# Performance work log

Measured on AMD Instinct MI355X. Metric: run time of the kernel, lower is better.

Reference implementation:

```python
import jax, jax.numpy as jnp
import numpy as np

B, N, DIM = 4, 4096, 1024
HEADS, DIM_HEAD = 16, 64
DIM_INNER = HEADS * DIM_HEAD
ATTN_SCALE = 8.0
EPS = 1e-12  # F.normalize default eps


def setup_inputs() -> dict:
    key = jax.random.key(0)
    k1, k2, k3, k4, k5 = jax.random.split(key, 5)
    x = jax.random.normal(k1, (B, N, DIM), dtype=jnp.float32)
    gamma = jnp.ones((DIM,), dtype=jnp.float32)
    # stored as (in, out) so forward is x @ w
    w_qkv = jax.random.normal(k2, (DIM, 3 * DIM_INNER), dtype=jnp.float32) * (DIM ** -0.5)
    temperature = jnp.ones((HEADS, 1, 1), dtype=jnp.float32)
    w_out = jax.random.normal(k3, (DIM_INNER, DIM), dtype=jnp.float32) * (DIM_INNER ** -0.5)
    return {"x": x, "gamma": gamma, "w_qkv": w_qkv, "temperature": temperature, "w_out": w_out}


def _l2norm(t):
    # F.normalize(t, dim=-1): t / max(||t||_2, eps)
    n = jnp.linalg.norm(t, axis=-1, keepdims=True)
    return t / jnp.maximum(n, EPS)


def reference(x, gamma, w_qkv, temperature, w_out):
    b, n, dim = x.shape
    # RMSNorm: F.normalize(x, dim=-1) * sqrt(dim) * gamma
    xn = _l2norm(x) * (dim ** 0.5) * gamma
    # QKV projection -> qkv b h d n
    qkv = (xn @ w_qkv).reshape(b, n, 3, HEADS, DIM_HEAD)
    qkv = qkv.transpose(2, 0, 3, 4, 1)  # (3, b, h, d, n)
    q, k, v = qkv[0], qkv[1], qkv[2]
    # l2-normalize q, k over the sequence (last) axis; temperature-scale q
    q = _l2norm(q) * jnp.exp(temperature)  # temperature: (h,1,1) broadcast
    k = _l2norm(k)
    # cross-covariance attention over the small channel dim d
    sim = jnp.einsum('bhdn,bhen->bhde', q, k) * ATTN_SCALE
    attn = jax.nn.softmax(sim, axis=-1)
    out = jnp.einsum('bhde,bhen->bhdn', attn, v)
    # b h d n -> b n (h d), then out projection
    out = out.transpose(0, 3, 1, 2).reshape(b, n, DIM_INNER)
    return out @ w_out
```

## Files before the change

### kernel.cpp

```cpp
#include <hip/hip_runtime.h>
#include <stdint.h>

typedef unsigned short u16;
typedef unsigned int u32;
typedef __attribute__((ext_vector_type(8))) __bf16 bf16x8;
typedef __attribute__((ext_vector_type(4))) float f32x4;

#define M_TOT 16384
#define DIMX  1024

__device__ __forceinline__ u16 f2b(float f) {
  u32 u = __builtin_bit_cast(u32, f);
  u32 r = (u + 0x7fffu + ((u >> 16) & 1u)) >> 16;
  return (u16)r;
}

__device__ __forceinline__ void gl2lds16(const void* g, void* l) {
  __builtin_amdgcn_global_load_lds((const __attribute__((address_space(1))) void*)g,
                                   (__attribute__((address_space(3))) void*)l,
                                   16, 0, 0);
}

__global__ __launch_bounds__(256) void k_rms(const float* __restrict__ x,
                                             const float* __restrict__ gamma,
                                             u16* __restrict__ xn) {
  int row = blockIdx.x;
  int t = threadIdx.x;
  const float4* xr = (const float4*)(x + (size_t)row * DIMX);
  float4 v = xr[t];
  float ss = v.x * v.x + v.y * v.y + v.z * v.z + v.w * v.w;
#pragma unroll
  for (int o = 32; o > 0; o >>= 1) ss += __shfl_xor(ss, o, 64);
  __shared__ float wss[4];
  int w = t >> 6;
  if ((t & 63) == 0) wss[w] = ss;
  __syncthreads();
  float tot = wss[0] + wss[1] + wss[2] + wss[3];
  float scale = 32.0f / fmaxf(sqrtf(tot), 1e-12f);
  float4 g = ((const float4*)gamma)[t];
  ushort4 o4;
  o4.x = f2b(v.x * scale * g.x);
  o4.y = f2b(v.y * scale * g.y);
  o4.z = f2b(v.z * scale * g.z);
  o4.w = f2b(v.w * scale * g.w);
  ((ushort4*)xn)[(size_t)row * 256 + t] = o4;
}

__global__ __launch_bounds__(256) void k_castT2(const float* __restrict__ wqkv,
                                                const float* __restrict__ wout,
                                                u16* __restrict__ wqT,
                                                u16* __restrict__ woT) {
  __shared__ float tile[32][33];
  const float* in; u16* out; int Cc; int c0;
  if (blockIdx.x < 96) { in = wqkv; out = wqT; Cc = 3072; c0 = blockIdx.x * 32; }
  else                 { in = wout; out = woT; Cc = 1024; c0 = (blockIdx.x - 96) * 32; }
  int r0 = blockIdx.y * 32;
  int tx = threadIdx.x, ty = threadIdx.y;
#pragma unroll
  for (int i = 0; i < 4; i++)
    tile[ty + i * 8][tx] = in[(size_t)(r0 + ty + i * 8) * Cc + c0 + tx];
  __syncthreads();
#pragma unroll
  for (int i = 0; i < 4; i++)
    out[(size_t)(c0 + ty + i * 8) * 1024 + r0 + tx] = f2b(tile[tx][ty + i * 8]);
}


template<bool SWAP>
__device__ __forceinline__ f32x4 mf(bf16x8 a, bf16x8 b, f32x4 c) {
  return SWAP ? __builtin_amdgcn_mfma_f32_16x16x32_bf16(b, a, c, 0, 0, 0)
              : __builtin_amdgcn_mfma_f32_16x16x32_bf16(a, b, c, 0, 0, 0);
}

__device__ __forceinline__ void stage_ab(const u16* __restrict__ Ag,
                                         const u16* __restrict__ Bg,
                                         u16* dstA, u16* dstB, int t, int k0) {
#pragma unroll
  for (int r = 0; r < 2; r++) {
    int c = r * 512 + t;
    int row = c >> 2, s = c & 3;
    int g = s ^ ((row >> 1) & 3);
    gl2lds16(Ag + (size_t)row * 1024 + k0 + g * 8,
             dstA + (r * 512 + (t >> 6) * 64) * 8);
  }
  {
    int row = t >> 2, s = t & 3;
    int g = s ^ ((row >> 1) & 3);
    gl2lds16(Bg + (size_t)row * 1024 + k0 + g * 8,
             dstB + ((t >> 6) * 64) * 8);
  }
}

template<bool SWAP>
__device__ __forceinline__ void gemm_core(const u16* __restrict__ Ag,
                                          const u16* __restrict__ Bg,
                                          u16* lds, int t, f32x4 (&acc)[4][4]) {
  const int lane = t & 63;
  const int r16 = lane & 15, q = lane >> 4;
  const int wr = (t >> 6) >> 1, wc = (t >> 6) & 1;
  const int arow = wr * 64 + r16;
  const int brow = wc * 64 + r16;

  stage_ab(Ag, Bg, lds, lds + 8192, t, 0);
  asm volatile("s_waitcnt vmcnt(0)" ::: "memory");
  __builtin_amdgcn_s_barrier();

  bf16x8 af[4], bf[4];
#pragma unroll 1
  for (int tt = 0; tt < 32; tt++) {
    const int cur = (tt & 1) ? 12288 : 0;
    const int nxt = cur ^ 12288;
    const int k1 = ((tt + 1) & 31) << 5;
    stage_ab(Ag, Bg, lds + nxt, lds + nxt + 8192, t, k1);
    const u16* A = lds + cur;
    const u16* B = lds + cur + 8192;
#pragma unroll
    for (int i = 0; i < 4; i++) {
      int ar = i * 16 + arow;
      int br = i * 16 + brow;
      af[i] = *(const bf16x8*)(A + ar * 32 + (q ^ ((ar >> 1) & 3)) * 8);
      bf[i] = *(const bf16x8*)(B + br * 32 + (q ^ ((br >> 1) & 3)) * 8);
    }
    __builtin_amdgcn_s_setprio(1);
#pragma unroll
    for (int i = 0; i < 4; i++)
#pragma unroll
      for (int j = 0; j < 4; j++)
        acc[i][j] = mf<SWAP>(af[i], bf[j], acc[i][j]);
    __builtin_amdgcn_s_setprio(0);
    asm volatile("s_waitcnt vmcnt(0)" ::: "memory");
    __builtin_amdgcn_s_barrier();
  }
}

__global__ __launch_bounds__(512, 4) void k_gemm1(const u16* __restrict__ A,
                                                  const u16* __restrict__ Bt,
                                                  u16* __restrict__ qkT,
                                                  u16* __restrict__ vmat,
                                                  float* __restrict__ sumsq) {
  __shared__ u16 lds[2 * 12288];
  int l = blockIdx.x;
  int xcd = l & 7, c = l >> 3;
  int mt = xcd * 8 + (c & 7);
  int nt = c >> 3;
  int m0 = mt * 256, n0 = nt * 128;
  int t = threadIdx.x, lane = t & 63;
  int r16 = lane & 15, q = lane >> 4;
  int wr = (t >> 6) >> 1, wc = (t >> 6) & 1;
  f32x4 acc[4][4] = {};
  if (n0 < 2048) {
    gemm_core<false>(A + (size_t)m0 * 1024, Bt + (size_t)n0 * 1024, lds, t, acc);
    int b = m0 >> 12;
#pragma unroll
    for (int j = 0; j < 4; j++) {
      int cc = n0 + wc * 64 + j * 16 + r16;
      float colss = 0.f;
#pragma unroll
      for (int i = 0; i < 4; i++) {
        f32x4 a = acc[i][j];
        colss += a.x * a.x + a.y * a.y + a.z * a.z + a.w * a.w;
        int m = m0 + wr * 64 + i * 16 + q * 4;
        ushort4 o4;
        o4.x = f2b(a.x); o4.y = f2b(a.y); o4.z = f2b(a.z); o4.w = f2b(a.w);
        *(ushort4*)(qkT + (size_t)cc * M_TOT + m) = o4;
      }
      colss += __shfl_xor(colss, 16, 64);
      colss += __shfl_xor(colss, 32, 64);
      if (lane < 16) atomicAdd(&sumsq[b * 2048 + cc], colss);
    }
  } else {
    gemm_core<true>(A + (size_t)m0 * 1024, Bt + (size_t)n0 * 1024, lds, t, acc);
    int vc0 = n0 - 2048;
#pragma unroll
    for (int i = 0; i < 4; i++) {
      int m = m0 + wr * 64 + i * 16 + r16;
#pragma unroll
      for (int j = 0; j < 4; j++) {
        int cc = vc0 + wc * 64 + j * 16 + q * 4;
        f32x4 a = acc[i][j];
        ushort4 o4;
        o4.x = f2b(a.x); o4.y = f2b(a.y); o4.z = f2b(a.z); o4.w = f2b(a.w);
        *(ushort4*)(vmat + (size_t)m * 1024 + cc) = o4;
      }
    }
  }
}

__global__ __launch_bounds__(256) void k_attn_s(const u16* __restrict__ qkT,
                                                float* __restrict__ Spart) {
  __shared__ u16 Ql[64 * 256];
  __shared__ u16 Kl[64 * 256];
  int bh = blockIdx.x, split = blockIdx.y;
  int b = bh >> 4, h = bh & 15;
  int t = threadIdx.x, lane = t & 63, w = t >> 6;
  int r16 = lane & 15, q = lane >> 4;
  const u16* qbase = qkT + (size_t)(h * 64) * M_TOT + b * 4096 + split * 1024;
  const u16* kbase = qkT + (size_t)(1024 + h * 64) * M_TOT + b * 4096 + split * 1024;
  int drow = w * 16 + r16;
  f32x4 acc[4] = {};
#pragma unroll 1
  for (int it = 0; it < 4; it++) {
    int ncol = it * 256;
#pragma unroll
    for (int r = 0; r < 8; r++) {
      int ch = r * 256 + t;
      int row = ch >> 5;
      int sl = (ch & 31) ^ (row & 31);
      gl2lds16(qbase + (size_t)row * M_TOT + ncol + sl * 8,
               Ql + (r * 256 + w * 64) * 8);
      gl2lds16(kbase + (size_t)row * M_TOT + ncol + sl * 8,
               Kl + (r * 256 + w * 64) * 8);
    }
    asm volatile("s_waitcnt vmcnt(0)" ::: "memory");
    __syncthreads();
#pragma unroll
    for (int it2 = 0; it2 < 8; it2++) {
      bf16x8 aq = *(const bf16x8*)(Ql + drow * 256 + (((it2 * 4 + q) ^ (drow & 31)) * 8));
#pragma unroll
      for (int j = 0; j < 4; j++) {
        int erow = j * 16 + r16;
        bf16x8 bk = *(const bf16x8*)(Kl + erow * 256 + (((it2 * 4 + q) ^ (erow & 31)) * 8));
        acc[j] = __builtin_amdgcn_mfma_f32_16x16x32_bf16(bk, aq, acc[j], 0, 0, 0);
      }
    }
    __syncthreads();
  }
  float* Sp = Spart + ((size_t)split * 64 + bh) * 4096;
#pragma unroll
  for (int j = 0; j < 4; j++)
    *(f32x4*)(Sp + drow * 64 + j * 16 + q * 4) = acc[j];
}

__global__ __launch_bounds__(256) void k_softmax(const float* __restrict__ Spart,
                                                 const float* __restrict__ sumsq,
                                                 const float* __restrict__ temp,
                                                 u16* __restrict__ PT) {
  int bh = blockIdx.x;
  int b = bh >> 4, h = bh & 15;
  int t = threadIdx.x;
  int d = t & 63, w = t >> 6;
  int e0 = w * 16;
  __shared__ float rnk[64];
  __shared__ float redm[4][64];
  __shared__ float reds[4][64];
  if (t < 64) rnk[t] = 1.0f / fmaxf(sqrtf(sumsq[b * 2048 + 1024 + h * 64 + t]), 1e-12f);
  __syncthreads();
  float nq = sqrtf(sumsq[b * 2048 + h * 64 + d]);
  float qs = 8.0f * __expf(temp[h]) / fmaxf(nq, 1e-12f);
  const float* Sp = Spart + (size_t)bh * 4096 + d * 64 + e0;
  float vals[16];
#pragma unroll
  for (int e = 0; e < 16; e += 4) {
    f32x4 v = {};
#pragma unroll
    for (int s = 0; s < 4; s++)
      v += *(const f32x4*)(Sp + (size_t)s * 64 * 4096 + e);
    vals[e + 0] = v.x; vals[e + 1] = v.y; vals[e + 2] = v.z; vals[e + 3] = v.w;
  }
  float mx = -3.0e38f;
#pragma unroll
  for (int e = 0; e < 16; e++) {
    float v = vals[e] * qs * rnk[e0 + e];
    vals[e] = v;
    mx = fmaxf(mx, v);
  }
  redm[w][d] = mx;
  __syncthreads();
  float M = fmaxf(fmaxf(redm[0][d], redm[1][d]), fmaxf(redm[2][d], redm[3][d]));
  float s = 0.f;
#pragma unroll
  for (int e = 0; e < 16; e++) {
    float v = __expf(vals[e] - M);
    vals[e] = v;
    s += v;
  }
  reds[w][d] = s;
  __syncthreads();
  float inv = 1.0f / (reds[0][d] + reds[1][d] + reds[2][d] + reds[3][d]);
#pragma unroll
  for (int e = 0; e < 16; e++)
    PT[((size_t)bh * 64 + e0 + e) * 64 + d] = f2b(vals[e] * inv);
}

__global__ __launch_bounds__(256) void k_m(const u16* __restrict__ woT,
                                           const u16* __restrict__ PT,
                                           u16* __restrict__ MT) {
  int bh = blockIdx.x;
  int b = bh >> 4, h = bh & 15;
  int o0 = blockIdx.y * 128;
  int t = threadIdx.x, lane = t & 63, w = t >> 6;
  int r16 = lane & 15, q = lane >> 4;
  const u16* pbase = PT + (size_t)bh * 4096;
  f32x4 acc[2][4] = {};
#pragma unroll
  for (int ks = 0; ks < 2; ks++) {
    int kk = ks * 32 + q * 8;
    bf16x8 af[2], bfr[4];
#pragma unroll
    for (int i = 0; i < 2; i++)
      af[i] = *(const bf16x8*)(woT + (size_t)(o0 + w * 32 + i * 16 + r16) * 1024 + h * 64 + kk);
#pragma unroll
    for (int j = 0; j < 4; j++)
      bfr[j] = *(const bf16x8*)(pbase + (size_t)(j * 16 + r16) * 64 + kk);
#pragma unroll
    for (int i = 0; i < 2; i++)
#pragma unroll
      for (int j = 0; j < 4; j++)
        acc[i][j] = __builtin_amdgcn_mfma_f32_16x16x32_bf16(af[i], bfr[j], acc[i][j], 0, 0, 0);
  }
  u16* dst = MT + (size_t)b * 1024 * 1024;
#pragma unroll
  for (int i = 0; i < 2; i++) {
    int o = o0 + w * 32 + i * 16 + q * 4;
#pragma unroll
    for (int j = 0; j < 4; j++) {
      int e = h * 64 + j * 16 + r16;
      f32x4 a = acc[i][j];
      dst[(size_t)(o + 0) * 1024 + e] = f2b(a.x);
      dst[(size_t)(o + 1) * 1024 + e] = f2b(a.y);
      dst[(size_t)(o + 2) * 1024 + e] = f2b(a.z);
      dst[(size_t)(o + 3) * 1024 + e] = f2b(a.w);
    }
  }
}

__global__ __launch_bounds__(512, 4) void k_gemm2(const u16* __restrict__ A,
                                                  const u16* __restrict__ Bt,
                                                  float* __restrict__ C) {
  __shared__ u16 lds[2 * 12288];
  int l = blockIdx.x;
  int xcd = l & 7, c = l >> 3;
  int mt = xcd * 8 + (c & 7);
  int nt = c >> 3;
  int m0 = mt * 256, n0 = nt * 128;
  int b = m0 >> 12;
  const u16* Bb = Bt + (size_t)b * 1024 * 1024;
  int t = threadIdx.x, lane = t & 63;
  int r16 = lane & 15, q = lane >> 4;
  int wr = (t >> 6) >> 1, wc = (t >> 6) & 1;
  f32x4 acc[4][4] = {};
  gemm_core<true>(A + (size_t)m0 * 1024, Bb + (size_t)n0 * 1024, lds, t, acc);
#pragma unroll
  for (int i = 0; i < 4; i++) {
    int m = m0 + wr * 64 + i * 16 + r16;
#pragma unroll
    for (int j = 0; j < 4; j++) {
      int cc = n0 + wc * 64 + j * 16 + q * 4;
      *(f32x4*)(C + (size_t)m * 1024 + cc) = acc[i][j];
    }
  }
}

extern "C" void kernel_launch(void* const* d_in, const int* in_sizes, int n_in,
                              void* d_out, int out_size, void* d_ws, size_t ws_size,
                              hipStream_t stream) {
  const float* x     = (const float*)d_in[0];
  const float* gamma = (const float*)d_in[1];
  const float* wqkv  = (const float*)d_in[2];
  const float* temp  = (const float*)d_in[3];
  const float* wout  = (const float*)d_in[4];
  float* out = (float*)d_out;

  char* ws = (char*)d_ws;
  size_t off = 0;
  u16* xn = (u16*)(ws + off);    off += (size_t)M_TOT * 1024 * 2;
  u16* wqT = (u16*)(ws + off);   off += (size_t)3072 * 1024 * 2;
  u16* woT = (u16*)(ws + off);   off += (size_t)1024 * 1024 * 2;
  u16* qkT = (u16*)(ws + off);   off += (size_t)2048 * M_TOT * 2;
  u16* vmat = (u16*)(ws + off);  off += (size_t)M_TOT * 1024 * 2;
  float* sumsq = (float*)(ws + off); off += (size_t)4 * 2048 * 4;
  u16* PT = (u16*)(ws + off);    off += (size_t)64 * 64 * 64 * 2;
  u16* MT = (u16*)(ws + off);    off += (size_t)4 * 1024 * 1024 * 2;

  float* Spart = (float*)xn;

  hipMemsetAsync((void*)sumsq, 0, (size_t)4 * 2048 * 4, stream);

  k_rms<<<16384, 256, 0, stream>>>(x, gamma, xn);
  dim3 cb(32, 8);
  k_castT2<<<dim3(128, 32), cb, 0, stream>>>(wqkv, wout, wqT, woT);
  k_gemm1<<<1536, 512, 0, stream>>>(xn, wqT, qkT, vmat, sumsq);
  k_attn_s<<<dim3(64, 4), 256, 0, stream>>>(qkT, Spart);
  k_softmax<<<64, 256, 0, stream>>>(Spart, sumsq, temp, PT);
  k_m<<<dim3(64, 8), 256, 0, stream>>>(woT, PT, MT);
  k_gemm2<<<512, 512, 0, stream>>>(vmat, MT, out);
}
```

Measured before the change: 326.3 us.

## Fuse all stages into one persistent kernel with grid-wide barriers

Replaces seven separate kernel launches with a single persistent 512-block kernel. Stages are separated by a software grid barrier, an atomic counter with spin-wait. The attention-score stage is re-split into 16 partial sums so all 512 blocks have work. Softmax and the P·Wout product are fused, keeping P in LDS instead of a global buffer. The aim is to remove launch gaps and tail effects between stages, at the cost of relying on all 512 blocks being co-resident, idle blocks during small stages, and a 3-tile-per-block loop for the first GEMM.

```diff
diff --git a/kernel.cpp b/kernel.cpp
--- a/kernel.cpp
+++ b/kernel.cpp
@@ -8,6 +8,7 @@
 
 #define M_TOT 16384
 #define DIMX  1024
+#define NBLK  512
 
 __device__ __forceinline__ u16 f2b(float f) {
   u32 u = __builtin_bit_cast(u32, f);
@@ -21,50 +22,16 @@
                                    16, 0, 0);
 }
 
-__global__ __launch_bounds__(256) void k_rms(const float* __restrict__ x,
-                                             const float* __restrict__ gamma,
-                                             u16* __restrict__ xn) {
-  int row = blockIdx.x;
-  int t = threadIdx.x;
-  const float4* xr = (const float4*)(x + (size_t)row * DIMX);
-  float4 v = xr[t];
-  float ss = v.x * v.x + v.y * v.y + v.z * v.z + v.w * v.w;
-#pragma unroll
-  for (int o = 32; o > 0; o >>= 1) ss += __shfl_xor(ss, o, 64);
-  __shared__ float wss[4];
-  int w = t >> 6;
-  if ((t & 63) == 0) wss[w] = ss;
+__device__ __forceinline__ void gsync(u32* cnt, u32 thresh) {
+  __threadfence();
   __syncthreads();
-  float tot = wss[0] + wss[1] + wss[2] + wss[3];
-  float scale = 32.0f / fmaxf(sqrtf(tot), 1e-12f);
-  float4 g = ((const float4*)gamma)[t];
-  ushort4 o4;
-  o4.x = f2b(v.x * scale * g.x);
-  o4.y = f2b(v.y * scale * g.y);
-  o4.z = f2b(v.z * scale * g.z);
-  o4.w = f2b(v.w * scale * g.w);
-  ((ushort4*)xn)[(size_t)row * 256 + t] = o4;
-}
-
-__global__ __launch_bounds__(256) void k_castT2(const float* __restrict__ wqkv,
-                                                const float* __restrict__ wout,
-                                                u16* __restrict__ wqT,
-                                                u16* __restrict__ woT) {
-  __shared__ float tile[32][33];
-  const float* in; u16* out; int Cc; int c0;
-  if (blockIdx.x < 96) { in = wqkv; out = wqT; Cc = 3072; c0 = blockIdx.x * 32; }
-  else                 { in = wout; out = woT; Cc = 1024; c0 = (blockIdx.x - 96) * 32; }
-  int r0 = blockIdx.y * 32;
-  int tx = threadIdx.x, ty = threadIdx.y;
-#pragma unroll
-  for (int i = 0; i < 4; i++)
-    tile[ty + i * 8][tx] = in[(size_t)(r0 + ty + i * 8) * Cc + c0 + tx];
+  if (threadIdx.x == 0) {
+    atomicAdd(cnt, 1u);
+    while (atomicAdd(cnt, 0u) < thresh) __builtin_amdgcn_s_sleep(2);
+  }
   __syncthreads();
-#pragma unroll
-  for (int i = 0; i < 4; i++)
-    out[(size_t)(c0 + ty + i * 8) * 1024 + r0 + tx] = f2b(tile[tx][ty + i * 8]);
-}
-
+  __threadfence();
+}
 
 template<bool SWAP>
 __device__ __forceinline__ f32x4 mf(bf16x8 a, bf16x8 b, f32x4 c) {
@@ -133,220 +100,276 @@
   }
 }
 
-__global__ __launch_bounds__(512, 4) void k_gemm1(const u16* __restrict__ A,
-                                                  const u16* __restrict__ Bt,
-                                                  u16* __restrict__ qkT,
-                                                  u16* __restrict__ vmat,
-                                                  float* __restrict__ sumsq) {
-  __shared__ u16 lds[2 * 12288];
-  int l = blockIdx.x;
-  int xcd = l & 7, c = l >> 3;
-  int mt = xcd * 8 + (c & 7);
-  int nt = c >> 3;
-  int m0 = mt * 256, n0 = nt * 128;
-  int t = threadIdx.x, lane = t & 63;
-  int r16 = lane & 15, q = lane >> 4;
-  int wr = (t >> 6) >> 1, wc = (t >> 6) & 1;
-  f32x4 acc[4][4] = {};
-  if (n0 < 2048) {
-    gemm_core<false>(A + (size_t)m0 * 1024, Bt + (size_t)n0 * 1024, lds, t, acc);
+__global__ __launch_bounds__(512, 4) void k_mega(
+    const float* __restrict__ x, const float* __restrict__ gamma,
+    const float* __restrict__ wqkv, const float* __restrict__ wout,
+    const float* __restrict__ temp,
+    u16* __restrict__ xn, u16* __restrict__ wqT, u16* __restrict__ woT,
+    u16* __restrict__ qkT, u16* __restrict__ vmat,
+    float* __restrict__ sumsq, u16* __restrict__ MT,
+    float* __restrict__ Spart, float* __restrict__ out, u32* cnt) {
+  __shared__ __align__(16) char smem[65536];
+  const int t = threadIdx.x;
+  const int blk = blockIdx.x;
+  const int lane = t & 63;
+  const int r16 = lane & 15, q = lane >> 4;
+
+  {
+    float* tile = (float*)smem;
+    float* wss  = (float*)(smem + 8448);
+    int vb = t >> 8;
+    int tl = t & 255;
+#pragma unroll 1
+    for (int i = 0; i < 20; i++) {
+      int v = blk * 2 + vb + i * 1024;
+      if (v < 16384) {
+        const float4* xr = (const float4*)(x + (size_t)v * DIMX);
+        float4 vv = xr[tl];
+        float ss = vv.x * vv.x + vv.y * vv.y + vv.z * vv.z + vv.w * vv.w;
+#pragma unroll
+        for (int o = 32; o > 0; o >>= 1) ss += __shfl_xor(ss, o, 64);
+        if ((tl & 63) == 0) wss[vb * 4 + (tl >> 6)] = ss;
+        __syncthreads();
+        float tot = wss[vb * 4 + 0] + wss[vb * 4 + 1] + wss[vb * 4 + 2] + wss[vb * 4 + 3];
+        float scale = 32.0f / fmaxf(sqrtf(tot), 1e-12f);
+        float4 g = ((const float4*)gamma)[tl];
+        ushort4 o4;
+        o4.x = f2b(vv.x * scale * g.x);
+        o4.y = f2b(vv.y * scale * g.y);
+        o4.z = f2b(vv.z * scale * g.z);
+        o4.w = f2b(vv.w * scale * g.w);
+        ((ushort4*)xn)[(size_t)v * 256 + tl] = o4;
+      } else {
+        int bb = v - 16384;
+        int bx = bb & 127, by = bb >> 7;
+        int r0 = by * 32;
+        int tx = tl & 31, ty = tl >> 5;
+        const float* in; u16* outp; int Cc, c0;
+        if (bx < 96) { in = wqkv; outp = wqT; Cc = 3072; c0 = bx * 32; }
+        else         { in = wout; outp = woT; Cc = 1024; c0 = (bx - 96) * 32; }
+        float* tl2 = tile + vb * 32 * 33;
+#pragma unroll
+        for (int i2 = 0; i2 < 4; i2++)
+          tl2[(ty + i2 * 8) * 33 + tx] = in[(size_t)(r0 + ty + i2 * 8) * Cc + c0 + tx];
+        __syncthreads();
+#pragma unroll
+        for (int i2 = 0; i2 < 4; i2++)
+          outp[(size_t)(c0 + ty + i2 * 8) * 1024 + r0 + tx] = f2b(tl2[tx * 33 + ty + i2 * 8]);
+      }
+      __syncthreads();
+    }
+  }
+  gsync(cnt, NBLK);
+
+  {
+    u16* lds = (u16*)smem;
+#pragma unroll 1
+    for (int i = 0; i < 3; i++) {
+      int l = blk + i * NBLK;
+      int xcd = l & 7, c = l >> 3;
+      int mt = xcd * 8 + (c & 7);
+      int nt = c >> 3;
+      int m0 = mt * 256, n0 = nt * 128;
+      int wr = (t >> 6) >> 1, wc = (t >> 6) & 1;
+      f32x4 acc[4][4] = {};
+      if (n0 < 2048) {
+        gemm_core<false>(xn + (size_t)m0 * 1024, wqT + (size_t)n0 * 1024, lds, t, acc);
+        int b = m0 >> 12;
+#pragma unroll
+        for (int j = 0; j < 4; j++) {
+          int cc = n0 + wc * 64 + j * 16 + r16;
+          float colss = 0.f;
+#pragma unroll
+          for (int i2 = 0; i2 < 4; i2++) {
+            f32x4 a = acc[i2][j];
+            colss += a.x * a.x + a.y * a.y + a.z * a.z + a.w * a.w;
+            int m = m0 + wr * 64 + i2 * 16 + q * 4;
+            ushort4 o4;
+            o4.x = f2b(a.x); o4.y = f2b(a.y); o4.z = f2b(a.z); o4.w = f2b(a.w);
+            *(ushort4*)(qkT + (size_t)cc * M_TOT + m) = o4;
+          }
+          colss += __shfl_xor(colss, 16, 64);
+          colss += __shfl_xor(colss, 32, 64);
+          if (lane < 16) atomicAdd(&sumsq[b * 2048 + cc], colss);
+        }
+      } else {
+        gemm_core<true>(xn + (size_t)m0 * 1024, wqT + (size_t)n0 * 1024, lds, t, acc);
+        int vc0 = n0 - 2048;
+#pragma unroll
+        for (int i2 = 0; i2 < 4; i2++) {
+          int m = m0 + wr * 64 + i2 * 16 + r16;
+#pragma unroll
+          for (int j = 0; j < 4; j++) {
+            int cc = vc0 + wc * 64 + j * 16 + q * 4;
+            f32x4 a = acc[i2][j];
+            ushort4 o4;
+            o4.x = f2b(a.x); o4.y = f2b(a.y); o4.z = f2b(a.z); o4.w = f2b(a.w);
+            *(ushort4*)(vmat + (size_t)m * 1024 + cc) = o4;
+          }
+        }
+      }
+    }
+  }
+  gsync(cnt, 2 * NBLK);
+
+  {
+    u16* Ql = (u16*)smem;
+    u16* Kl = (u16*)smem + 16384;
+    int bh = blk & 63, split = blk >> 6;
+    int b = bh >> 4, h = bh & 15;
+    int w = t >> 6, wl = w & 3, wg = w >> 2;
+    const u16* qbase = qkT + (size_t)(h * 64) * M_TOT + b * 4096 + split * 512;
+    const u16* kbase = qkT + (size_t)(1024 + h * 64) * M_TOT + b * 4096 + split * 512;
+    int drow = wl * 16 + r16;
+    f32x4 acc[4] = {};
+#pragma unroll 1
+    for (int it = 0; it < 2; it++) {
+      int ncol = it * 256;
+#pragma unroll
+      for (int r = 0; r < 4; r++) {
+        int ch = r * 512 + t;
+        int row = ch >> 5;
+        int sl = (ch & 31) ^ (row & 31);
+        gl2lds16(qbase + (size_t)row * M_TOT + ncol + sl * 8,
+                 Ql + (r * 512 + w * 64) * 8);
+        gl2lds16(kbase + (size_t)row * M_TOT + ncol + sl * 8,
+                 Kl + (r * 512 + w * 64) * 8);
+      }
+      asm volatile("s_waitcnt vmcnt(0)" ::: "memory");
+      __syncthreads();
+#pragma unroll
+      for (int h2 = 0; h2 < 4; h2++) {
+        int it2 = h2 * 2 + wg;
+        bf16x8 aq = *(const bf16x8*)(Ql + drow * 256 + (((it2 * 4 + q) ^ (drow & 31)) * 8));
+#pragma unroll
+        for (int j = 0; j < 4; j++) {
+          int erow = j * 16 + r16;
+          bf16x8 bk = *(const bf16x8*)(Kl + erow * 256 + (((it2 * 4 + q) ^ (erow & 31)) * 8));
+          acc[j] = __builtin_amdgcn_mfma_f32_16x16x32_bf16(bk, aq, acc[j], 0, 0, 0);
+        }
+      }
+      __syncthreads();
+    }
+    int sp = split * 2 + wg;
+    float* Sp = Spart + ((size_t)sp * 64 + bh) * 4096;
+#pragma unroll
+    for (int j = 0; j < 4; j++)
+      *(f32x4*)(Sp + drow * 64 + j * 16 + q * 4) = acc[j];
+  }
+  gsync(cnt, 3 * NBLK);
+
+  if (blk < 64) {
+    u16* PT_lds = (u16*)smem;
+    float* rnk  = (float*)(smem + 8192);
+    float* redm = (float*)(smem + 8448);
+    float* reds = (float*)(smem + 10496);
+    int bh = blk;
+    int b = bh >> 4, h = bh & 15;
+    int d = t & 63, w = t >> 6;
+    int e0 = w * 8;
+    if (t < 64) rnk[t] = 1.0f / fmaxf(sqrtf(sumsq[b * 2048 + 1024 + h * 64 + t]), 1e-12f);
+    __syncthreads();
+    float nq = sqrtf(sumsq[b * 2048 + h * 64 + d]);
+    float qs = 8.0f * __expf(temp[h]) / fmaxf(nq, 1e-12f);
+    float vals[8];
+#pragma unroll
+    for (int e = 0; e < 8; e += 4) {
+      f32x4 v = {};
+#pragma unroll
+      for (int s = 0; s < 16; s++)
+        v += *(const f32x4*)(Spart + ((size_t)s * 64 + bh) * 4096 + d * 64 + e0 + e);
+      vals[e + 0] = v.x; vals[e + 1] = v.y; vals[e + 2] = v.z; vals[e + 3] = v.w;
+    }
+    float mx = -3.0e38f;
+#pragma unroll
+    for (int e = 0; e < 8; e++) {
+      float v = vals[e] * qs * rnk[e0 + e];
+      vals[e] = v;
+      mx = fmaxf(mx, v);
+    }
+    redm[w * 64 + d] = mx;
+    __syncthreads();
+    float M = redm[d];
+#pragma unroll
+    for (int k = 1; k < 8; k++) M = fmaxf(M, redm[k * 64 + d]);
+    float ssum = 0.f;
+#pragma unroll
+    for (int e = 0; e < 8; e++) {
+      float v = __expf(vals[e] - M);
+      vals[e] = v;
+      ssum += v;
+    }
+    reds[w * 64 + d] = ssum;
+    __syncthreads();
+    float tot = reds[d];
+#pragma unroll
+    for (int k = 1; k < 8; k++) tot += reds[k * 64 + d];
+    float inv = 1.0f / tot;
+#pragma unroll
+    for (int e = 0; e < 8; e++)
+      PT_lds[(e0 + e) * 64 + d] = f2b(vals[e] * inv);
+    __syncthreads();
+    int tl = t & 255, vb = t >> 8;
+    int lane2 = tl & 63, w4 = tl >> 6;
+    int r2 = lane2 & 15, q2 = lane2 >> 4;
+    u16* dst = MT + (size_t)b * 1024 * 1024;
+#pragma unroll 1
+    for (int ot = vb; ot < 8; ot += 2) {
+      int o0 = ot * 128;
+      f32x4 acc2[2][4] = {};
+#pragma unroll
+      for (int ks = 0; ks < 2; ks++) {
+        int kk = ks * 32 + q2 * 8;
+        bf16x8 af[2], bfr[4];
+#pragma unroll
+        for (int i = 0; i < 2; i++)
+          af[i] = *(const bf16x8*)(woT + (size_t)(o0 + w4 * 32 + i * 16 + r2) * 1024 + h * 64 + kk);
+#pragma unroll
+        for (int j = 0; j < 4; j++)
+          bfr[j] = *(const bf16x8*)(PT_lds + (size_t)(j * 16 + r2) * 64 + kk);
+#pragma unroll
+        for (int i = 0; i < 2; i++)
+#pragma unroll
+          for (int j = 0; j < 4; j++)
+            acc2[i][j] = __builtin_amdgcn_mfma_f32_16x16x32_bf16(af[i], bfr[j], acc2[i][j], 0, 0, 0);
+      }
+#pragma unroll
+      for (int i = 0; i < 2; i++) {
+        int o = o0 + w4 * 32 + i * 16 + q2 * 4;
+#pragma unroll
+        for (int j = 0; j < 4; j++) {
+          int e = h * 64 + j * 16 + r2;
+          f32x4 a = acc2[i][j];
+          dst[(size_t)(o + 0) * 1024 + e] = f2b(a.x);
+          dst[(size_t)(o + 1) * 1024 + e] = f2b(a.y);
+          dst[(size_t)(o + 2) * 1024 + e] = f2b(a.z);
+          dst[(size_t)(o + 3) * 1024 + e] = f2b(a.w);
+        }
+      }
+    }
+  }
+  gsync(cnt, 4 * NBLK);
+
+  {
+    u16* lds = (u16*)smem;
+    int l = blk;
+    int xcd = l & 7, c = l >> 3;
+    int mt = xcd * 8 + (c & 7);
+    int nt = c >> 3;
+    int m0 = mt * 256, n0 = nt * 128;
     int b = m0 >> 12;
-#pragma unroll
-    for (int j = 0; j < 4; j++) {
-      int cc = n0 + wc * 64 + j * 16 + r16;
-      float colss = 0.f;
-#pragma unroll
-      for (int i = 0; i < 4; i++) {
-        f32x4 a = acc[i][j];
-        colss += a.x * a.x + a.y * a.y + a.z * a.z + a.w * a.w;
-        int m = m0 + wr * 64 + i * 16 + q * 4;
-        ushort4 o4;
-        o4.x = f2b(a.x); o4.y = f2b(a.y); o4.z = f2b(a.z); o4.w = f2b(a.w);
-        *(ushort4*)(qkT + (size_t)cc * M_TOT + m) = o4;
-      }
-      colss += __shfl_xor(colss, 16, 64);
-      colss += __shfl_xor(colss, 32, 64);
-      if (lane < 16) atomicAdd(&sumsq[b * 2048 + cc], colss);
-    }
-  } else {
-    gemm_core<true>(A + (size_t)m0 * 1024, Bt + (size_t)n0 * 1024, lds, t, acc);
-    int vc0 = n0 - 2048;
+    int wr = (t >> 6) >> 1, wc = (t >> 6) & 1;
+    f32x4 acc[4][4] = {};
+    gemm_core<true>(vmat + (size_t)m0 * 1024,
+                    MT + (size_t)b * 1048576 + (size_t)n0 * 1024, lds, t, acc);
 #pragma unroll
     for (int i = 0; i < 4; i++) {
       int m = m0 + wr * 64 + i * 16 + r16;
 #pragma unroll
       for (int j = 0; j < 4; j++) {
-        int cc = vc0 + wc * 64 + j * 16 + q * 4;
-        f32x4 a = acc[i][j];
-        ushort4 o4;
-        o4.x = f2b(a.x); o4.y = f2b(a.y); o4.z = f2b(a.z); o4.w = f2b(a.w);
-        *(ushort4*)(vmat + (size_t)m * 1024 + cc) = o4;
-      }
-    }
-  }
-}
-
-__global__ __launch_bounds__(256) void k_attn_s(const u16* __restrict__ qkT,
-                                                float* __restrict__ Spart) {
-  __shared__ u16 Ql[64 * 256];
-  __shared__ u16 Kl[64 * 256];
-  int bh = blockIdx.x, split = blockIdx.y;
-  int b = bh >> 4, h = bh & 15;
-  int t = threadIdx.x, lane = t & 63, w = t >> 6;
-  int r16 = lane & 15, q = lane >> 4;
-  const u16* qbase = qkT + (size_t)(h * 64) * M_TOT + b * 4096 + split * 1024;
-  const u16* kbase = qkT + (size_t)(1024 + h * 64) * M_TOT + b * 4096 + split * 1024;
-  int drow = w * 16 + r16;
-  f32x4 acc[4] = {};
-#pragma unroll 1
-  for (int it = 0; it < 4; it++) {
-    int ncol = it * 256;
-#pragma unroll
-    for (int r = 0; r < 8; r++) {
-      int ch = r * 256 + t;
-      int row = ch >> 5;
-      int sl = (ch & 31) ^ (row & 31);
-      gl2lds16(qbase + (size_t)row * M_TOT + ncol + sl * 8,
-               Ql + (r * 256 + w * 64) * 8);
-      gl2lds16(kbase + (size_t)row * M_TOT + ncol + sl * 8,
-               Kl + (r * 256 + w * 64) * 8);
-    }
-    asm volatile("s_waitcnt vmcnt(0)" ::: "memory");
-    __syncthreads();
-#pragma unroll
-    for (int it2 = 0; it2 < 8; it2++) {
-      bf16x8 aq = *(const bf16x8*)(Ql + drow * 256 + (((it2 * 4 + q) ^ (drow & 31)) * 8));
-#pragma unroll
-      for (int j = 0; j < 4; j++) {
-        int erow = j * 16 + r16;
-        bf16x8 bk = *(const bf16x8*)(Kl + erow * 256 + (((it2 * 4 + q) ^ (erow & 31)) * 8));
-        acc[j] = __builtin_amdgcn_mfma_f32_16x16x32_bf16(bk, aq, acc[j], 0, 0, 0);
-      }
-    }
-    __syncthreads();
-  }
-  float* Sp = Spart + ((size_t)split * 64 + bh) * 4096;
-#pragma unroll
-  for (int j = 0; j < 4; j++)
-    *(f32x4*)(Sp + drow * 64 + j * 16 + q * 4) = acc[j];
-}
-
-__global__ __launch_bounds__(256) void k_softmax(const float* __restrict__ Spart,
-                                                 const float* __restrict__ sumsq,
-                                                 const float* __restrict__ temp,
-                                                 u16* __restrict__ PT) {
-  int bh = blockIdx.x;
-  int b = bh >> 4, h = bh & 15;
-  int t = threadIdx.x;
-  int d = t & 63, w = t >> 6;
-  int e0 = w * 16;
-  __shared__ float rnk[64];
-  __shared__ float redm[4][64];
-  __shared__ float reds[4][64];
-  if (t < 64) rnk[t] = 1.0f / fmaxf(sqrtf(sumsq[b * 2048 + 1024 + h * 64 + t]), 1e-12f);
-  __syncthreads();
-  float nq = sqrtf(sumsq[b * 2048 + h * 64 + d]);
-  float qs = 8.0f * __expf(temp[h]) / fmaxf(nq, 1e-12f);
-  const float* Sp = Spart + (size_t)bh * 4096 + d * 64 + e0;
-  float vals[16];
-#pragma unroll
-  for (int e = 0; e < 16; e += 4) {
-    f32x4 v = {};
-#pragma unroll
-    for (int s = 0; s < 4; s++)
-      v += *(const f32x4*)(Sp + (size_t)s * 64 * 4096 + e);
-    vals[e + 0] = v.x; vals[e + 1] = v.y; vals[e + 2] = v.z; vals[e + 3] = v.w;
-  }
-  float mx = -3.0e38f;
-#pragma unroll
-  for (int e = 0; e < 16; e++) {
-    float v = vals[e] * qs * rnk[e0 + e];
-    vals[e] = v;
-    mx = fmaxf(mx, v);
-  }
-  redm[w][d] = mx;
-  __syncthreads();
-  float M = fmaxf(fmaxf(redm[0][d], redm[1][d]), fmaxf(redm[2][d], redm[3][d]));
-  float s = 0.f;
-#pragma unroll
-  for (int e = 0; e < 16; e++) {
-    float v = __expf(vals[e] - M);
-    vals[e] = v;
-    s += v;
-  }
-  reds[w][d] = s;
-  __syncthreads();
-  float inv = 1.0f / (reds[0][d] + reds[1][d] + reds[2][d] + reds[3][d]);
-#pragma unroll
-  for (int e = 0; e < 16; e++)
-    PT[((size_t)bh * 64 + e0 + e) * 64 + d] = f2b(vals[e] * inv);
-}
-
-__global__ __launch_bounds__(256) void k_m(const u16* __restrict__ woT,
-                                           const u16* __restrict__ PT,
-                                           u16* __restrict__ MT) {
-  int bh = blockIdx.x;
-  int b = bh >> 4, h = bh & 15;
-  int o0 = blockIdx.y * 128;
-  int t = threadIdx.x, lane = t & 63, w = t >> 6;
-  int r16 = lane & 15, q = lane >> 4;
-  const u16* pbase = PT + (size_t)bh * 4096;
-  f32x4 acc[2][4] = {};
-#pragma unroll
-  for (int ks = 0; ks < 2; ks++) {
-    int kk = ks * 32 + q * 8;
-    bf16x8 af[2], bfr[4];
-#pragma unroll
-    for (int i = 0; i < 2; i++)
-      af[i] = *(const bf16x8*)(woT + (size_t)(o0 + w * 32 + i * 16 + r16) * 1024 + h * 64 + kk);
-#pragma unroll
-    for (int j = 0; j < 4; j++)
-      bfr[j] = *(const bf16x8*)(pbase + (size_t)(j * 16 + r16) * 64 + kk);
-#pragma unroll
-    for (int i = 0; i < 2; i++)
-#pragma unroll
-      for (int j = 0; j < 4; j++)
-        acc[i][j] = __builtin_amdgcn_mfma_f32_16x16x32_bf16(af[i], bfr[j], acc[i][j], 0, 0, 0);
-  }
-  u16* dst = MT + (size_t)b * 1024 * 1024;
-#pragma unroll
-  for (int i = 0; i < 2; i++) {
-    int o = o0 + w * 32 + i * 16 + q * 4;
-#pragma unroll
-    for (int j = 0; j < 4; j++) {
-      int e = h * 64 + j * 16 + r16;
-      f32x4 a = acc[i][j];
-      dst[(size_t)(o + 0) * 1024 + e] = f2b(a.x);
-      dst[(size_t)(o + 1) * 1024 + e] = f2b(a.y);
-      dst[(size_t)(o + 2) * 1024 + e] = f2b(a.z);
-      dst[(size_t)(o + 3) * 1024 + e] = f2b(a.w);
-    }
-  }
-}
-
-__global__ __launch_bounds__(512, 4) void k_gemm2(const u16* __restrict__ A,
-                                                  const u16* __restrict__ Bt,
-                                                  float* __restrict__ C) {
-  __shared__ u16 lds[2 * 12288];
-  int l = blockIdx.x;
-  int xcd = l & 7, c = l >> 3;
-  int mt = xcd * 8 + (c & 7);
-  int nt = c >> 3;
-  int m0 = mt * 256, n0 = nt * 128;
-  int b = m0 >> 12;
-  const u16* Bb = Bt + (size_t)b * 1024 * 1024;
-  int t = threadIdx.x, lane = t & 63;
-  int r16 = lane & 15, q = lane >> 4;
-  int wr = (t >> 6) >> 1, wc = (t >> 6) & 1;
-  f32x4 acc[4][4] = {};
-  gemm_core<true>(A + (size_t)m0 * 1024, Bb + (size_t)n0 * 1024, lds, t, acc);
-#pragma unroll
-  for (int i = 0; i < 4; i++) {
-    int m = m0 + wr * 64 + i * 16 + r16;
-#pragma unroll
-    for (int j = 0; j < 4; j++) {
-      int cc = n0 + wc * 64 + j * 16 + q * 4;
-      *(f32x4*)(C + (size_t)m * 1024 + cc) = acc[i][j];
+        int cc = n0 + wc * 64 + j * 16 + q * 4;
+        *(f32x4*)(out + (size_t)m * 1024 + cc) = acc[i][j];
+      }
     }
   }
 }
@@ -369,19 +392,14 @@
   u16* qkT = (u16*)(ws + off);   off += (size_t)2048 * M_TOT * 2;
   u16* vmat = (u16*)(ws + off);  off += (size_t)M_TOT * 1024 * 2;
   float* sumsq = (float*)(ws + off); off += (size_t)4 * 2048 * 4;
-  u16* PT = (u16*)(ws + off);    off += (size_t)64 * 64 * 64 * 2;
+  u32* cnt = (u32*)(ws + off);   off += 64;
   u16* MT = (u16*)(ws + off);    off += (size_t)4 * 1024 * 1024 * 2;
 
   float* Spart = (float*)xn;
 
-  hipMemsetAsync((void*)sumsq, 0, (size_t)4 * 2048 * 4, stream);
-
-  k_rms<<<16384, 256, 0, stream>>>(x, gamma, xn);
-  dim3 cb(32, 8);
-  k_castT2<<<dim3(128, 32), cb, 0, stream>>>(wqkv, wout, wqT, woT);
-  k_gemm1<<<1536, 512, 0, stream>>>(xn, wqT, qkT, vmat, sumsq);
-  k_attn_s<<<dim3(64, 4), 256, 0, stream>>>(qkT, Spart);
-  k_softmax<<<64, 256, 0, stream>>>(Spart, sumsq, temp, PT);
-  k_m<<<dim3(64, 8), 256, 0, stream>>>(woT, PT, MT);
-  k_gemm2<<<512, 512, 0, stream>>>(vmat, MT, out);
-}
+  hipMemsetAsync((void*)sumsq, 0, (size_t)4 * 2048 * 4 + 64, stream);
+
+  k_mega<<<NBLK, 512, 0, stream>>>(x, gamma, wqkv, wout, temp,
+                                   xn, wqT, woT, qkT, vmat,
+                                   sumsq, MT, Spart, out, cnt);
+}
```

After: 1.111 ms. 241% more time.
